# Performance work log

Hardware: AMD Instinct MI355X
Metric: run time of the kernel (lower is better)

## Reference

```python
import jax, jax.numpy as jnp
import numpy as np
from jax import lax

NSTEPS = 4
STEPSIZE = 0.1


def setup_inputs() -> dict:
    key = jax.random.key(0)
    k1, k2, k3, k4 = jax.random.split(key, 4)
    B, N, D = 8, 40962, 40  # batch, n_patch, d_latent+d_ancillary
    H, D_DYN = 512, 32
    x = jax.random.normal(k1, (B, N, D), dtype=jnp.float32)
    # stencil: self + 3 neighbours per dual-mesh vertex
    nbrs = jax.random.randint(k2, (N, 3), 0, N, dtype=jnp.int32)
    index = jnp.concatenate([jnp.arange(N, dtype=jnp.int32)[:, None], nbrs], axis=1)  # (N,4)
    W1 = jax.random.normal(k3, (4, D, H), dtype=jnp.float32) * (1.0 / np.sqrt(4 * D))
    b1 = jnp.zeros((H,), dtype=jnp.float32)
    W2 = jax.random.normal(k4, (H, D_DYN), dtype=jnp.float32) * (1.0 / np.sqrt(H))
    b2 = jnp.zeros((D_DYN,), dtype=jnp.float32)
    return {"x": x, "index": index, "W1": W1, "b1": b1, "W2": W2, "b2": b2}


def interaction_model(z, W1, b1, W2, b2):
    # z: (B, N, 4, D) -> (B, N, d_dyn); MLP over flattened 4-vertex stencil
    h = jax.nn.gelu(jnp.einsum('bnkd,kdh->bnh', z, W1) + b1)
    return h @ W2 + b2


def reference(x, index, W1, b1, W2, b2):
    D = x.shape[-1]
    d_dyn = W2.shape[-1]

    def step(x, _):
        z = x[:, index, :]                       # (B, N, 4, D) gather of 4-neighbour stencil
        fz = interaction_model(z, W1, b1, W2, b2)  # (B, N, d_dyn)
        dx = jnp.pad(fz, ((0, 0), (0, 0), (0, D - d_dyn)))  # ancillary channels untouched
        return x + STEPSIZE * dx, None

    x, _ = lax.scan(step, x, None, length=NSTEPS)
    return x
```

## Files before the change

kernel.cpp:

```cpp
#include <hip/hip_runtime.h>
#include <math.h>

constexpr int BB   = 8;
constexpr int NN   = 40962;
constexpr int DDIM = 40;
constexpr int HH   = 512;
constexpr int DDYN = 32;
constexpr float STEPSZ = 0.1f;

constexpr int TM   = 64;
constexpr int NTHR = 1024;
constexpr int ZS   = 168;

constexpr size_t X_ELEMS = (size_t)BB * NN * DDIM;
constexpr size_t X_BYTES = X_ELEMS * 4;
constexpr int W1P_ELEMS = 32 * 5 * 64 * 8;
constexpr int W2P_BYTES = 2 * 16 * 64 * 8;

constexpr int Z_BYTES = TM * ZS * 2;
constexpr int H_OFF   = Z_BYTES;
constexpr int H_BYTES = TM * HH;
constexpr int XS_OFF  = H_OFF + H_BYTES;
constexpr int LDS_TOT = XS_OFF + TM * DDIM * 4;

typedef __attribute__((ext_vector_type(8))) short short8;
typedef __attribute__((ext_vector_type(4))) float f32x4;
typedef __attribute__((ext_vector_type(4))) unsigned short u16x4;

__device__ __forceinline__ unsigned short bf16_rne(float f) {
    unsigned int u = __float_as_uint(f);
    return (unsigned short)((u + 0x7FFFu + ((u >> 16) & 1u)) >> 16);
}

__device__ __forceinline__ unsigned int cvt_pk_bf16(float lo, float hi) {
    unsigned int r;
    asm("v_cvt_pk_bf16_f32 %0, %1, %2" : "=v"(r) : "v"(lo), "v"(hi));
    return r;
}

__device__ __forceinline__ float exp2_hw(float x) {
    float r;
    asm("v_exp_f32 %0, %1" : "=v"(r) : "v"(x));
    return r;
}

__device__ __forceinline__ unsigned char f32_to_fp8_sw(float f) {
    if (!(f == f)) return 0x7f;
    unsigned u = __float_as_uint(f);
    unsigned s = (u >> 24) & 0x80u;
    float a = fabsf(f);
    if (a >= 464.f) return (unsigned char)(s | 0x7e);
    int e = (int)((u >> 23) & 0xff) - 127;
    if (e < -6) {
        int q = (int)fminf(fmaxf(a * 512.0f + 0.5f, 0.f), 7.f);
        return (unsigned char)(s | q);
    }
    unsigned m = u & 0x7fffffu;
    unsigned keep = m >> 20, rest = m & 0xfffffu;
    keep += (rest > 0x80000u || (rest == 0x80000u && (keep & 1u))) ? 1u : 0u;
    if (keep == 8u) { keep = 0u; ++e; if (e > 8) return (unsigned char)(s | 0x7e); }
    return (unsigned char)(s | ((unsigned)(e + 7) << 3) | keep);
}

__device__ __forceinline__ unsigned int pk4_fp8(float a, float b, float c, float d) {
#if __has_builtin(__builtin_amdgcn_cvt_pk_fp8_f32)
    int r = __builtin_amdgcn_cvt_pk_fp8_f32(a, b, 0, false);
    r     = __builtin_amdgcn_cvt_pk_fp8_f32(c, d, r, true);
    return (unsigned int)r;
#else
    return (unsigned)f32_to_fp8_sw(a) | ((unsigned)f32_to_fp8_sw(b) << 8) |
           ((unsigned)f32_to_fp8_sw(c) << 16) | ((unsigned)f32_to_fp8_sw(d) << 24);
#endif
}

__device__ __forceinline__ float gelu_fast(float x) {
    float u = x * fmaf(0.044715f, x * x, 1.0f);
    float e = exp2_hw(-2.30220817f * u);
    return x * __builtin_amdgcn_rcpf(1.0f + e);
}

__global__ __launch_bounds__(256) void pack_w1(const float* __restrict__ W1,
                                               unsigned short* __restrict__ W1p) {
    int t = blockIdx.x * 256 + threadIdx.x;
    if (t >= W1P_ELEMS) return;
    int j = t & 7, ln = (t >> 3) & 63, g = t >> 9;
    int kk = g % 5, mt = g / 5;
    int nl = ln & 15, q = ln >> 4;
    int k = kk * 32 + q * 8 + j, m = mt * 16 + nl;
    W1p[t] = bf16_rne(W1[(size_t)k * HH + m]);
}
__global__ __launch_bounds__(256) void pack_w2_fp8(const float* __restrict__ W2,
                                                   unsigned char* __restrict__ W2p) {
    int t = blockIdx.x * 256 + threadIdx.x;
    if (t >= W2P_BYTES) return;
    int j = t & 7, ln = (t >> 3) & 63, g = t >> 9;
    int kk = g & 15, jt = g >> 4;
    int nl = ln & 15, q = ln >> 4;
    int k = kk * 32 + q * 8 + j, m = jt * 16 + nl;
    float v = W2[(size_t)k * DDYN + m];
#if __has_builtin(__builtin_amdgcn_cvt_pk_fp8_f32)
    W2p[t] = (unsigned char)(__builtin_amdgcn_cvt_pk_fp8_f32(v, v, 0, false) & 0xff);
#else
    W2p[t] = f32_to_fp8_sw(v);
#endif
}

__global__ __launch_bounds__(NTHR, 8) void step_mfma(
    const float* __restrict__ xsrc, float* __restrict__ xdst,
    const int* __restrict__ index,
    const unsigned short* __restrict__ W1p, const float* __restrict__ b1,
    const unsigned char* __restrict__ W2p, const float* __restrict__ b2)
{
    __shared__ alignas(16) unsigned char smem[LDS_TOT];
    unsigned short* z = (unsigned short*)smem;
    unsigned char*  h = smem + H_OFF;
    float* xself = (float*)(smem + XS_OFF);
    float* fz0 = (float*)smem;
    float* fz1 = (float*)(smem + TM * 36 * 4);

    const int tid = threadIdx.x;
    const int w   = tid >> 6;
    const int ln  = tid & 63;
    const int nl  = ln & 15;
    const int q   = ln >> 4;
    const int n0  = blockIdx.x * TM;
    const int b   = blockIdx.y;
    const size_t xbase = (size_t)b * NN * DDIM;

    for (int e = tid; e < TM * 4 * 10; e += NTHR) {
        int m = e / 40, r = e - m * 40;
        int k = r / 10, qq = r - k * 10;
        unsigned int lo = 0, hi = 0;
        int n = n0 + m;
        if (n < NN) {
            int nb = index[n * 4 + k];
            float4 v = ((const float4*)(xsrc + xbase + (size_t)nb * DDIM))[qq];
            lo = cvt_pk_bf16(v.x, v.y);
            hi = cvt_pk_bf16(v.z, v.w);
            if (k == 0) *(float4*)(xself + m * 40 + qq * 4) = v;
        }
        *(uint2*)(z + m * ZS + k * 40 + qq * 4) = make_uint2(lo, hi);
    }
    __syncthreads();

    f32x4 acc[2][4];
    #pragma unroll
    for (int i = 0; i < 2; ++i) {
        float4 bv = *(const float4*)(b1 + (w * 2 + i) * 16 + q * 4);
        f32x4 a; a[0] = bv.x; a[1] = bv.y; a[2] = bv.z; a[3] = bv.w;
        #pragma unroll
        for (int nt = 0; nt < 4; ++nt) acc[i][nt] = a;
    }
    #pragma unroll
    for (int kk = 0; kk < 5; ++kk) {
        short8 afr0 = *(const short8*)(W1p + (size_t)(((w * 2 + 0) * 5 + kk) * 512 + ln * 8));
        short8 afr1 = *(const short8*)(W1p + (size_t)(((w * 2 + 1) * 5 + kk) * 512 + ln * 8));
        #pragma unroll
        for (int nt = 0; nt < 4; ++nt) {
            short8 bfr = *(const short8*)(z + (nt * 16 + nl) * ZS + kk * 32 + q * 8);
            acc[0][nt] = __builtin_amdgcn_mfma_f32_16x16x32_bf16(afr0, bfr, acc[0][nt], 0, 0, 0);
            acc[1][nt] = __builtin_amdgcn_mfma_f32_16x16x32_bf16(afr1, bfr, acc[1][nt], 0, 0, 0);
        }
    }
    __syncthreads();

    #pragma unroll
    for (int i = 0; i < 2; ++i) {
        const int hid  = (w * 2 + i) * 16 + q * 4;
        const int sub8 = hid >> 3;
        const int o4   = (q & 1) << 2;
        #pragma unroll
        for (int nt = 0; nt < 4; ++nt) {
            f32x4 a = acc[i][nt];
            unsigned int p = pk4_fp8(gelu_fast(a[0]), gelu_fast(a[1]),
                                     gelu_fast(a[2]), gelu_fast(a[3]));
            int node = nt * 16 + nl;
            *(unsigned int*)(h + node * 512 + ((sub8 ^ (node & 7)) << 3) + o4) = p;
        }
    }
    __syncthreads();

    const int nt2 = w & 3;
    const int jt  = (w >> 2) & 1;
    const int kh  = (w >> 3) & 1;
    const int hrow = nt2 * 16 + nl;
    f32x4 acc2;
    if (kh == 0) {
        float4 bv = *(const float4*)(b2 + jt * 16 + q * 4);
        acc2[0] = bv.x; acc2[1] = bv.y; acc2[2] = bv.z; acc2[3] = bv.w;
    } else {
        acc2[0] = acc2[1] = acc2[2] = acc2[3] = 0.f;
    }
    #pragma unroll
    for (int kk = 0; kk < 8; ++kk) {
        int kg = kh * 8 + kk;
        long long afr, bfr;
        __builtin_memcpy(&afr, W2p + (size_t)(((jt * 16 + kg) * 64 + ln) * 8), 8);
        __builtin_memcpy(&bfr, h + hrow * 512 + (((kg * 4 + q) ^ (hrow & 7)) << 3), 8);
        acc2 = __builtin_amdgcn_mfma_f32_16x16x32_fp8_fp8(afr, bfr, acc2, 0, 0, 0);
    }
    {
        float* fzk = kh ? fz1 : fz0;
        *(f32x4*)(fzk + hrow * 36 + jt * 16 + q * 4) = acc2;
    }
    __syncthreads();

    if (tid < TM * 10) {
        int m = tid / 10, p = tid - m * 10;
        int n = n0 + m;
        if (n < NN) {
            float4 v = *(const float4*)(xself + m * 40 + p * 4);
            if (p < 8) {
                f32x4 f0 = *(const f32x4*)(fz0 + m * 36 + p * 4);
                f32x4 f1 = *(const f32x4*)(fz1 + m * 36 + p * 4);
                v.x = fmaf(STEPSZ, f0[0] + f1[0], v.x);
                v.y = fmaf(STEPSZ, f0[1] + f1[1], v.y);
                v.z = fmaf(STEPSZ, f0[2] + f1[2], v.z);
                v.w = fmaf(STEPSZ, f0[3] + f1[3], v.w);
            }
            *(float4*)(xdst + xbase + (size_t)n * DDIM + p * 4) = v;
        }
    }
}

constexpr int FTM = 16;
__device__ __forceinline__ float gelu_f(float x) { return gelu_fast(x); }
__global__ __launch_bounds__(256) void step_f32(
    const float* __restrict__ xsrc, float* __restrict__ xdst,
    const int* __restrict__ index,
    const float* __restrict__ W1, const float* __restrict__ b1,
    const float* __restrict__ W2, const float* __restrict__ b2)
{
    __shared__ float z_lds[FTM][160];
    __shared__ float h_lds[FTM][HH];
    __shared__ float fz_lds[FTM][DDYN];
    const int tid = threadIdx.x, tile = blockIdx.x, b = blockIdx.y;
    const int n0 = tile * FTM;
    const int nvalid = min(FTM, NN - n0);
    for (int e = tid; e < FTM * 4 * 10; e += 256) {
        int m = e / 40, r = e % 40, k = r / 10, qq = r % 10;
        float4 v = make_float4(0.f, 0.f, 0.f, 0.f);
        int n = n0 + m;
        if (n < NN) {
            int nb = index[n * 4 + k];
            v = ((const float4*)(xsrc + ((size_t)b * NN + nb) * DDIM))[qq];
        }
        ((float4*)&z_lds[m][k * DDIM])[qq] = v;
    }
    __syncthreads();
    const int c0 = 2 * tid;
    float2 acc[FTM];
    {
        float bx = b1[c0], by = b1[c0 + 1];
        #pragma unroll
        for (int m = 0; m < FTM; ++m) { acc[m].x = bx; acc[m].y = by; }
    }
    for (int kd = 0; kd < 160; kd += 4) {
        float2 w0 = *(const float2*)(W1 + (size_t)(kd + 0) * HH + c0);
        float2 w1 = *(const float2*)(W1 + (size_t)(kd + 1) * HH + c0);
        float2 w2 = *(const float2*)(W1 + (size_t)(kd + 2) * HH + c0);
        float2 w3 = *(const float2*)(W1 + (size_t)(kd + 3) * HH + c0);
        #pragma unroll
        for (int m = 0; m < FTM; ++m) {
            float4 zv = *(const float4*)&z_lds[m][kd];
            acc[m].x = fmaf(zv.x, w0.x, acc[m].x); acc[m].y = fmaf(zv.x, w0.y, acc[m].y);
            acc[m].x = fmaf(zv.y, w1.x, acc[m].x); acc[m].y = fmaf(zv.y, w1.y, acc[m].y);
            acc[m].x = fmaf(zv.z, w2.x, acc[m].x); acc[m].y = fmaf(zv.z, w2.y, acc[m].y);
            acc[m].x = fmaf(zv.w, w3.x, acc[m].x); acc[m].y = fmaf(zv.w, w3.y, acc[m].y);
        }
    }
    #pragma unroll
    for (int m = 0; m < FTM; ++m) {
        h_lds[m][c0]     = gelu_f(acc[m].x);
        h_lds[m][c0 + 1] = gelu_f(acc[m].y);
    }
    __syncthreads();
    {
        const int j = tid & 31, mg = tid >> 5;
        float a0 = b2[j], a1 = a0;
        for (int c = 0; c < HH; c += 4) {
            float wa = W2[(size_t)(c + 0) * DDYN + j];
            float wb = W2[(size_t)(c + 1) * DDYN + j];
            float wc = W2[(size_t)(c + 2) * DDYN + j];
            float wd = W2[(size_t)(c + 3) * DDYN + j];
            float4 h0 = *(const float4*)&h_lds[mg][c];
            float4 h1 = *(const float4*)&h_lds[mg + 8][c];
            a0 = fmaf(h0.x, wa, a0); a0 = fmaf(h0.y, wb, a0);
            a0 = fmaf(h0.z, wc, a0); a0 = fmaf(h0.w, wd, a0);
            a1 = fmaf(h1.x, wa, a1); a1 = fmaf(h1.y, wb, a1);
            a1 = fmaf(h1.z, wc, a1); a1 = fmaf(h1.w, wd, a1);
        }
        fz_lds[mg][j] = a0; fz_lds[mg + 8][j] = a1;
    }
    __syncthreads();
    const size_t base = ((size_t)b * NN + n0) * (size_t)DDIM;
    for (int e = tid; e < nvalid * DDIM; e += 256) {
        int m = e / DDIM, d = e % DDIM;
        float v = xsrc[base + e];
        if (d < DDYN) v = fmaf(STEPSZ, fz_lds[m][d], v);
        xdst[base + e] = v;
    }
}

extern "C" void kernel_launch(void* const* d_in, const int* in_sizes, int n_in,
                              void* d_out, int out_size, void* d_ws, size_t ws_size,
                              hipStream_t stream) {
    const float* x   = (const float*)d_in[0];
    const int*   idx = (const int*)  d_in[1];
    const float* W1  = (const float*)d_in[2];
    const float* b1  = (const float*)d_in[3];
    const float* W2  = (const float*)d_in[4];
    const float* b2  = (const float*)d_in[5];
    float* out  = (float*)d_out;
    float* xbuf = (float*)d_ws;

    const size_t need = X_BYTES + (size_t)W1P_ELEMS * 2 + W2P_BYTES;
    if (ws_size >= need) {
        unsigned short* W1p = (unsigned short*)((char*)d_ws + X_BYTES);
        unsigned char*  W2p = (unsigned char*)(W1p + W1P_ELEMS);
        pack_w1<<<(W1P_ELEMS + 255) / 256, 256, 0, stream>>>(W1, W1p);
        pack_w2_fp8<<<(W2P_BYTES + 255) / 256, 256, 0, stream>>>(W2, W2p);
        dim3 grid((NN + TM - 1) / TM, BB), block(NTHR);
        step_mfma<<<grid, block, 0, stream>>>(x,    xbuf, idx, W1p, b1, W2p, b2);
        step_mfma<<<grid, block, 0, stream>>>(xbuf, out,  idx, W1p, b1, W2p, b2);
        step_mfma<<<grid, block, 0, stream>>>(out,  xbuf, idx, W1p, b1, W2p, b2);
        step_mfma<<<grid, block, 0, stream>>>(xbuf, out,  idx, W1p, b1, W2p, b2);
    } else {
        dim3 grid((NN + FTM - 1) / FTM, BB), block(256);
        step_f32<<<grid, block, 0, stream>>>(x,    xbuf, idx, W1, b1, W2, b2);
        step_f32<<<grid, block, 0, stream>>>(xbuf, out,  idx, W1, b1, W2, b2);
        step_f32<<<grid, block, 0, stream>>>(out,  xbuf, idx, W1, b1, W2, b2);
        step_f32<<<grid, block, 0, stream>>>(xbuf, out,  idx, W1, b1, W2, b2);
    }
}
```

Measured before the change: 647.1 us.

## Restructure MLP step: fused second GEMM epilogue, prefetching, cheaper GELU, skip static writes

After: 655.4 us. About the same (+1.3%).

```diff
diff --git a/kernel.cpp b/kernel.cpp
--- a/kernel.cpp
+++ b/kernel.cpp
@@ -25,7 +25,6 @@
 
 typedef __attribute__((ext_vector_type(8))) short short8;
 typedef __attribute__((ext_vector_type(4))) float f32x4;
-typedef __attribute__((ext_vector_type(4))) unsigned short u16x4;
 
 __device__ __forceinline__ unsigned short bf16_rne(float f) {
     unsigned int u = __float_as_uint(f);
@@ -73,10 +72,26 @@
 #endif
 }
 
-__device__ __forceinline__ float gelu_fast(float x) {
-    float u = x * fmaf(0.044715f, x * x, 1.0f);
-    float e = exp2_hw(-2.30220817f * u);
-    return x * __builtin_amdgcn_rcpf(1.0f + e);
+__device__ __forceinline__ f32x4 gelu4(f32x4 a) {
+    float d0, d1, d2, d3;
+    {
+        float t0 = a[0] * fmaf(-0.10294357f, a[0] * a[0], -2.3022077f);
+        float t1 = a[1] * fmaf(-0.10294357f, a[1] * a[1], -2.3022077f);
+        float t2 = a[2] * fmaf(-0.10294357f, a[2] * a[2], -2.3022077f);
+        float t3 = a[3] * fmaf(-0.10294357f, a[3] * a[3], -2.3022077f);
+        d0 = 1.0f + exp2_hw(t0);
+        d1 = 1.0f + exp2_hw(t1);
+        d2 = 1.0f + exp2_hw(t2);
+        d3 = 1.0f + exp2_hw(t3);
+    }
+    float r01 = __builtin_amdgcn_rcpf(d0 * d1);
+    float r23 = __builtin_amdgcn_rcpf(d2 * d3);
+    f32x4 g;
+    g[0] = a[0] * d1 * r01;
+    g[1] = a[1] * d0 * r01;
+    g[2] = a[2] * d3 * r23;
+    g[3] = a[3] * d2 * r23;
+    return g;
 }
 
 __global__ __launch_bounds__(256) void pack_w1(const float* __restrict__ W1,
@@ -109,14 +124,13 @@
     const float* __restrict__ xsrc, float* __restrict__ xdst,
     const int* __restrict__ index,
     const unsigned short* __restrict__ W1p, const float* __restrict__ b1,
-    const unsigned char* __restrict__ W2p, const float* __restrict__ b2)
+    const unsigned char* __restrict__ W2p, const float* __restrict__ b2,
+    int write_static)
 {
     __shared__ alignas(16) unsigned char smem[LDS_TOT];
     unsigned short* z = (unsigned short*)smem;
     unsigned char*  h = smem + H_OFF;
     float* xself = (float*)(smem + XS_OFF);
-    float* fz0 = (float*)smem;
-    float* fz1 = (float*)(smem + TM * 36 * 4);
 
     const int tid = threadIdx.x;
     const int w   = tid >> 6;
@@ -127,20 +141,43 @@
     const int b   = blockIdx.y;
     const size_t xbase = (size_t)b * NN * DDIM;
 
-    for (int e = tid; e < TM * 4 * 10; e += NTHR) {
-        int m = e / 40, r = e - m * 40;
-        int k = r / 10, qq = r - k * 10;
-        unsigned int lo = 0, hi = 0;
-        int n = n0 + m;
-        if (n < NN) {
-            int nb = index[n * 4 + k];
+    if (n0 + TM <= NN) {
+        for (int e = tid; e < TM * 4 * 10; e += NTHR) {
+            int m = e / 40, r = e - m * 40;
+            int k = r / 10, qq = r - k * 10;
+            int nb = index[(n0 + m) * 4 + k];
             float4 v = ((const float4*)(xsrc + xbase + (size_t)nb * DDIM))[qq];
-            lo = cvt_pk_bf16(v.x, v.y);
-            hi = cvt_pk_bf16(v.z, v.w);
-            if (k == 0) *(float4*)(xself + m * 40 + qq * 4) = v;
-        }
-        *(uint2*)(z + m * ZS + k * 40 + qq * 4) = make_uint2(lo, hi);
-    }
+            unsigned lo = cvt_pk_bf16(v.x, v.y);
+            unsigned hi = cvt_pk_bf16(v.z, v.w);
+            *(uint2*)(z + m * ZS + k * 40 + qq * 4) = make_uint2(lo, hi);
+            if (k == 0) {
+                int c = (qq < 8) ? (qq ^ (m & 7)) : qq;
+                *(float4*)(xself + m * 40 + c * 4) = v;
+            }
+        }
+    } else {
+        for (int e = tid; e < TM * 4 * 10; e += NTHR) {
+            int m = e / 40, r = e - m * 40;
+            int k = r / 10, qq = r - k * 10;
+            unsigned lo = 0, hi = 0;
+            int n = n0 + m;
+            float4 v = make_float4(0.f, 0.f, 0.f, 0.f);
+            if (n < NN) {
+                int nb = index[n * 4 + k];
+                v = ((const float4*)(xsrc + xbase + (size_t)nb * DDIM))[qq];
+                lo = cvt_pk_bf16(v.x, v.y);
+                hi = cvt_pk_bf16(v.z, v.w);
+            }
+            *(uint2*)(z + m * ZS + k * 40 + qq * 4) = make_uint2(lo, hi);
+            if (k == 0) {
+                int c = (qq < 8) ? (qq ^ (m & 7)) : qq;
+                *(float4*)(xself + m * 40 + c * 4) = v;
+            }
+        }
+    }
+    const unsigned short* w1b = W1p + ((size_t)(w * 2) * 5) * 512 + ln * 8;
+    short8 pf0 = *(const short8*)(w1b);
+    short8 pf1 = *(const short8*)(w1b + 5 * 512);
     __syncthreads();
 
     f32x4 acc[2][4];
@@ -151,18 +188,22 @@
         #pragma unroll
         for (int nt = 0; nt < 4; ++nt) acc[i][nt] = a;
     }
+    short8 afr0 = pf0, afr1 = pf1;
     #pragma unroll
     for (int kk = 0; kk < 5; ++kk) {
-        short8 afr0 = *(const short8*)(W1p + (size_t)(((w * 2 + 0) * 5 + kk) * 512 + ln * 8));
-        short8 afr1 = *(const short8*)(W1p + (size_t)(((w * 2 + 1) * 5 + kk) * 512 + ln * 8));
+        short8 na0, na1;
+        if (kk < 4) {
+            na0 = *(const short8*)(w1b + (kk + 1) * 512);
+            na1 = *(const short8*)(w1b + (5 + kk + 1) * 512);
+        }
         #pragma unroll
         for (int nt = 0; nt < 4; ++nt) {
             short8 bfr = *(const short8*)(z + (nt * 16 + nl) * ZS + kk * 32 + q * 8);
             acc[0][nt] = __builtin_amdgcn_mfma_f32_16x16x32_bf16(afr0, bfr, acc[0][nt], 0, 0, 0);
             acc[1][nt] = __builtin_amdgcn_mfma_f32_16x16x32_bf16(afr1, bfr, acc[1][nt], 0, 0, 0);
         }
-    }
-    __syncthreads();
+        afr0 = na0; afr1 = na1;
+    }
 
     #pragma unroll
     for (int i = 0; i < 2; ++i) {
@@ -171,60 +212,74 @@
         const int o4   = (q & 1) << 2;
         #pragma unroll
         for (int nt = 0; nt < 4; ++nt) {
-            f32x4 a = acc[i][nt];
-            unsigned int p = pk4_fp8(gelu_fast(a[0]), gelu_fast(a[1]),
-                                     gelu_fast(a[2]), gelu_fast(a[3]));
+            f32x4 g = gelu4(acc[i][nt]);
+            unsigned int p = pk4_fp8(g[0], g[1], g[2], g[3]);
             int node = nt * 16 + nl;
-            *(unsigned int*)(h + node * 512 + ((sub8 ^ (node & 7)) << 3) + o4) = p;
-        }
-    }
-    __syncthreads();
-
-    const int nt2 = w & 3;
-    const int jt  = (w >> 2) & 1;
-    const int kh  = (w >> 3) & 1;
-    const int hrow = nt2 * 16 + nl;
-    f32x4 acc2;
-    if (kh == 0) {
-        float4 bv = *(const float4*)(b2 + jt * 16 + q * 4);
-        acc2[0] = bv.x; acc2[1] = bv.y; acc2[2] = bv.z; acc2[3] = bv.w;
-    } else {
-        acc2[0] = acc2[1] = acc2[2] = acc2[3] = 0.f;
-    }
-    #pragma unroll
-    for (int kk = 0; kk < 8; ++kk) {
-        int kg = kh * 8 + kk;
-        long long afr, bfr;
-        __builtin_memcpy(&afr, W2p + (size_t)(((jt * 16 + kg) * 64 + ln) * 8), 8);
-        __builtin_memcpy(&bfr, h + hrow * 512 + (((kg * 4 + q) ^ (hrow & 7)) << 3), 8);
-        acc2 = __builtin_amdgcn_mfma_f32_16x16x32_fp8_fp8(afr, bfr, acc2, 0, 0, 0);
-    }
-    {
-        float* fzk = kh ? fz1 : fz0;
-        *(f32x4*)(fzk + hrow * 36 + jt * 16 + q * 4) = acc2;
-    }
-    __syncthreads();
-
-    if (tid < TM * 10) {
-        int m = tid / 10, p = tid - m * 10;
-        int n = n0 + m;
+            *(unsigned int*)(h + node * 512 + ((sub8 ^ (node & 15)) << 3) + o4) = p;
+        }
+    }
+
+    long long pa0 = 0, pa1 = 0;
+    if (w < 4) {
+        __builtin_memcpy(&pa0, W2p + (size_t)((0 * 64 + ln) * 8), 8);
+        __builtin_memcpy(&pa1, W2p + (size_t)(((16) * 64 + ln) * 8), 8);
+    }
+    __syncthreads();
+
+    if (w < 4) {
+        const int hrow = w * 16 + nl;
+        f32x4 acc2[2];
+        #pragma unroll
+        for (int jt = 0; jt < 2; ++jt) {
+            float4 bv = *(const float4*)(b2 + jt * 16 + q * 4);
+            acc2[jt][0] = bv.x; acc2[jt][1] = bv.y; acc2[jt][2] = bv.z; acc2[jt][3] = bv.w;
+        }
+        long long a0 = pa0, a1 = pa1;
+        #pragma unroll
+        for (int kg = 0; kg < 16; ++kg) {
+            long long n0a, n1a;
+            if (kg < 15) {
+                __builtin_memcpy(&n0a, W2p + (size_t)(((kg + 1) * 64 + ln) * 8), 8);
+                __builtin_memcpy(&n1a, W2p + (size_t)(((16 + kg + 1) * 64 + ln) * 8), 8);
+            }
+            long long bfr;
+            __builtin_memcpy(&bfr, h + hrow * 512 + (((kg * 4 + q) ^ (hrow & 15)) << 3), 8);
+            acc2[0] = __builtin_amdgcn_mfma_f32_16x16x32_fp8_fp8(a0, bfr, acc2[0], 0, 0, 0);
+            acc2[1] = __builtin_amdgcn_mfma_f32_16x16x32_fp8_fp8(a1, bfr, acc2[1], 0, 0, 0);
+            a0 = n0a; a1 = n1a;
+        }
+        int n = n0 + hrow;
         if (n < NN) {
-            float4 v = *(const float4*)(xself + m * 40 + p * 4);
-            if (p < 8) {
-                f32x4 f0 = *(const f32x4*)(fz0 + m * 36 + p * 4);
-                f32x4 f1 = *(const f32x4*)(fz1 + m * 36 + p * 4);
-                v.x = fmaf(STEPSZ, f0[0] + f1[0], v.x);
-                v.y = fmaf(STEPSZ, f0[1] + f1[1], v.y);
-                v.z = fmaf(STEPSZ, f0[2] + f1[2], v.z);
-                v.w = fmaf(STEPSZ, f0[3] + f1[3], v.w);
-            }
-            *(float4*)(xdst + xbase + (size_t)n * DDIM + p * 4) = v;
+            #pragma unroll
+            for (int jt = 0; jt < 2; ++jt) {
+                int c = (jt * 4 + q) ^ (hrow & 7);
+                float4 s = *(const float4*)(xself + hrow * 40 + c * 4);
+                float4 o;
+                o.x = fmaf(STEPSZ, acc2[jt][0], s.x);
+                o.y = fmaf(STEPSZ, acc2[jt][1], s.y);
+                o.z = fmaf(STEPSZ, acc2[jt][2], s.z);
+                o.w = fmaf(STEPSZ, acc2[jt][3], s.w);
+                *(float4*)(xdst + xbase + (size_t)n * DDIM + jt * 16 + q * 4) = o;
+            }
+        }
+    } else if (write_static) {
+        int t2 = tid - 256;
+        if (t2 < TM * 2) {
+            int m = t2 >> 1, qq = 8 + (t2 & 1);
+            int n = n0 + m;
+            if (n < NN) {
+                float4 v = *(const float4*)(xself + m * 40 + qq * 4);
+                *(float4*)(xdst + xbase + (size_t)n * DDIM + qq * 4) = v;
+            }
         }
     }
 }
 
 constexpr int FTM = 16;
-__device__ __forceinline__ float gelu_f(float x) { return gelu_fast(x); }
+__device__ __forceinline__ float gelu_f(float x) {
+    float t = x * fmaf(-0.10294357f, x * x, -2.3022077f);
+    return x * __builtin_amdgcn_rcpf(1.0f + exp2_hw(t));
+}
 __global__ __launch_bounds__(256) void step_f32(
     const float* __restrict__ xsrc, float* __restrict__ xdst,
     const int* __restrict__ index,
@@ -321,10 +376,10 @@
         pack_w1<<<(W1P_ELEMS + 255) / 256, 256, 0, stream>>>(W1, W1p);
         pack_w2_fp8<<<(W2P_BYTES + 255) / 256, 256, 0, stream>>>(W2, W2p);
         dim3 grid((NN + TM - 1) / TM, BB), block(NTHR);
-        step_mfma<<<grid, block, 0, stream>>>(x,    xbuf, idx, W1p, b1, W2p, b2);
-        step_mfma<<<grid, block, 0, stream>>>(xbuf, out,  idx, W1p, b1, W2p, b2);
-        step_mfma<<<grid, block, 0, stream>>>(out,  xbuf, idx, W1p, b1, W2p, b2);
-        step_mfma<<<grid, block, 0, stream>>>(xbuf, out,  idx, W1p, b1, W2p, b2);
+        step_mfma<<<grid, block, 0, stream>>>(x,    xbuf, idx, W1p, b1, W2p, b2, 1);
+        step_mfma<<<grid, block, 0, stream>>>(xbuf, out,  idx, W1p, b1, W2p, b2, 1);
+        step_mfma<<<grid, block, 0, stream>>>(out,  xbuf, idx, W1p, b1, W2p, b2, 0);
+        step_mfma<<<grid, block, 0, stream>>>(xbuf, out,  idx, W1p, b1, W2p, b2, 0);
     } else {
         dim3 grid((NN + FTM - 1) / FTM, BB), block(256);
         step_f32<<<grid, block, 0, stream>>>(x,    xbuf, idx, W1, b1, W2, b2);
```
